# Kernel optimization log

Hardware: AMD Instinct MI355X
Metric: run time of the kernel (lower is better)

Reference implementation:

```python
import jax, jax.numpy as jnp
import numpy as np

KNN = 10       # knn_size
TOPK = 4       # top_k_select
H = 4          # num_heads
HID = 64       # edge-MLP hidden dim


def setup_inputs() -> dict:
    key = jax.random.key(0)
    ks = jax.random.split(key, 12)
    B, V, D = 4, 4096, 256
    s = 0.02
    return {
        "voxel_tokens": jax.random.normal(ks[0], (B, V, D), jnp.float32),
        "voxel_coords": jax.random.uniform(ks[1], (B, V, 3), jnp.float32) * 10.0,
        "mask": jnp.ones((B, V), dtype=bool),
        # EdgeScoringMLP: Linear(2D+3 -> 64), Linear(64 -> 1)
        "W1": jax.random.normal(ks[2], (2 * D + 3, HID), jnp.float32) * s,
        "b1": jnp.zeros((HID,), jnp.float32),
        "W2": jax.random.normal(ks[3], (HID, 1), jnp.float32) * s,
        "b2": jnp.zeros((1,), jnp.float32),
        # CrossAttention projections (D -> D)
        "Wq": jax.random.normal(ks[4], (D, D), jnp.float32) * s,
        "bq": jnp.zeros((D,), jnp.float32),
        "Wk": jax.random.normal(ks[5], (D, D), jnp.float32) * s,
        "bk": jnp.zeros((D,), jnp.float32),
        "Wv": jax.random.normal(ks[6], (D, D), jnp.float32) * s,
        "bv": jnp.zeros((D,), jnp.float32),
        "Wo": jax.random.normal(ks[7], (D, D), jnp.float32) * s,
        "bo": jnp.zeros((D,), jnp.float32),
    }


def reference(voxel_tokens, voxel_coords, mask,
              W1, b1, W2, b2, Wq, bq, Wk, bk, Wv, bv, Wo, bo):
    # mask is all-True (Vp == V per batch element), so the original per-batch
    # loop over dynamic voxel counts is an exact vmap over B. Dropouts are in
    # eval mode (identity).
    D = voxel_tokens.shape[-1]
    Dh = D // H

    def single(tok, coo):  # tok: (V, D), coo: (V, 3)
        # --- KNN graph build (squared euclidean; monotonic in true cdist) ---
        sq = jnp.sum(coo * coo, axis=-1)                        # (V,)
        d2 = sq[:, None] + sq[None, :] - 2.0 * (coo @ coo.T)    # (V, V)
        _, knn = jax.lax.top_k(-d2, KNN + 1)                    # smallest dists
        knn = knn[:, 1:]                                        # drop self, (V, KNN)

        # --- edge features: [anchor_tok, neighbor_tok, rel_pos] ---
        nb_tok = tok[knn]                                       # (V, KNN, D)
        rel = coo[knn] - coo[:, None, :]                        # (V, KNN, 3)
        anchor = jnp.broadcast_to(tok[:, None, :], nb_tok.shape)
        ef = jnp.concatenate([anchor, nb_tok, rel], axis=-1)    # (V, KNN, 2D+3)

        # --- edge-MLP scoring + softmax + top-k edge select ---
        sc = (jax.nn.relu(ef @ W1 + b1) @ W2 + b2)[..., 0]      # (V, KNN)
        aw = jax.nn.softmax(sc, axis=-1)
        _, loc = jax.lax.top_k(aw, TOPK)                        # (V, TOPK)
        sel = jnp.take_along_axis(knn, loc, axis=-1)            # (V, TOPK)
        nbr = tok[sel]                                          # (V, TOPK, D)

        # --- cross attention over selected neighbors ---
        Q = (tok @ Wq + bq).reshape(-1, H, Dh)                  # (V, H, Dh)
        K = (nbr @ Wk + bk).reshape(-1, TOPK, H, Dh)            # (V, TOPK, H, Dh)
        Vv = (nbr @ Wv + bv).reshape(-1, TOPK, H, Dh)
        att = jnp.einsum('vhd,vshd->vhs', Q, K) / jnp.sqrt(jnp.float32(Dh))
        w = jax.nn.softmax(att, axis=-1)                        # (V, H, TOPK)
        out = jnp.einsum('vhs,vshd->vhd', w, Vv).reshape(-1, D)
        return out @ Wo + bo                                    # (V, D)

    return jax.vmap(single)(voxel_tokens, voxel_coords)        # (B, V, D)
```

## Files before the change

### kernel.cpp

```cpp
#include <hip/hip_runtime.h>
#include <hip/hip_bf16.h>

#define VV 4096
#define DDIM 256
#define KNN_K 10
#define TK 4

__device__ __forceinline__ float f_sq3(float x, float y, float z) {
    return __fadd_rn(__fadd_rn(__fmul_rn(x, x), __fmul_rn(y, y)), __fmul_rn(z, z));
}
__device__ __forceinline__ float f_dot3(float ax, float ay, float az,
                                        float bx, float by, float bz) {
    float d = __fmul_rn(ax, bx);
    d = __fmaf_rn(ay, by, d);
    d = __fmaf_rn(az, bz, d);
    return d;
}

__device__ __forceinline__ unsigned long long mkkey(float d2, int j) {
    unsigned u = __float_as_uint(d2);
    u ^= (unsigned)((int)u >> 31) | 0x80000000u;
    return ((unsigned long long)u << 32) | (unsigned)j;
}

__global__ void __launch_bounds__(256) an_gemm_kernel(
    const float* __restrict__ tok,
    const float* __restrict__ W1,
    const float* __restrict__ coords,
    float* __restrict__ AN,
    float4* __restrict__ cxyzs)
{
    __shared__ float As[16][68];
    __shared__ float Bs[16][68];

    const int mBlock = blockIdx.x * 64;
    const int grp    = blockIdx.y;
    const float* W   = W1 + (size_t)grp * 256 * 64;

    const int tid = threadIdx.x;

    if (grp == 0 && tid < 64) {
        int m = mBlock + tid;
        float x = coords[m * 3 + 0], y = coords[m * 3 + 1], z = coords[m * 3 + 2];
        cxyzs[m] = make_float4(x, y, z, f_sq3(x, y, z));
    }

    const int tx = tid & 15;
    const int ty = tid >> 4;

    const int ar  = tid >> 2;
    const int ac4 = tid & 3;
    const int br  = tid >> 4;
    const int bc4 = tid & 15;

    float acc[4][4] = {};

    for (int k0 = 0; k0 < 256; k0 += 16) {
        float4 a4 = *(const float4*)&tok[(size_t)(mBlock + ar) * 256 + k0 + ac4 * 4];
        As[ac4 * 4 + 0][ar] = a4.x;
        As[ac4 * 4 + 1][ar] = a4.y;
        As[ac4 * 4 + 2][ar] = a4.z;
        As[ac4 * 4 + 3][ar] = a4.w;
        float4 b4 = *(const float4*)&W[(size_t)(k0 + br) * 64 + bc4 * 4];
        *(float4*)&Bs[br][bc4 * 4] = b4;
        __syncthreads();
        #pragma unroll
        for (int kk = 0; kk < 16; kk++) {
            float4 av = *(const float4*)&As[kk][ty * 4];
            float4 bv4 = *(const float4*)&Bs[kk][tx * 4];
            acc[0][0] = fmaf(av.x, bv4.x, acc[0][0]); acc[0][1] = fmaf(av.x, bv4.y, acc[0][1]);
            acc[0][2] = fmaf(av.x, bv4.z, acc[0][2]); acc[0][3] = fmaf(av.x, bv4.w, acc[0][3]);
            acc[1][0] = fmaf(av.y, bv4.x, acc[1][0]); acc[1][1] = fmaf(av.y, bv4.y, acc[1][1]);
            acc[1][2] = fmaf(av.y, bv4.z, acc[1][2]); acc[1][3] = fmaf(av.y, bv4.w, acc[1][3]);
            acc[2][0] = fmaf(av.z, bv4.x, acc[2][0]); acc[2][1] = fmaf(av.z, bv4.y, acc[2][1]);
            acc[2][2] = fmaf(av.z, bv4.z, acc[2][2]); acc[2][3] = fmaf(av.z, bv4.w, acc[2][3]);
            acc[3][0] = fmaf(av.w, bv4.x, acc[3][0]); acc[3][1] = fmaf(av.w, bv4.y, acc[3][1]);
            acc[3][2] = fmaf(av.w, bv4.z, acc[3][2]); acc[3][3] = fmaf(av.w, bv4.w, acc[3][3]);
        }
        __syncthreads();
    }

    #pragma unroll
    for (int i = 0; i < 4; i++) {
        int m = mBlock + ty * 4 + i;
        float4 o;
        o.x = acc[i][0]; o.y = acc[i][1]; o.z = acc[i][2]; o.w = acc[i][3];
        *(float4*)&AN[(size_t)m * 128 + grp * 64 + tx * 4] = o;
    }
}

__global__ void __launch_bounds__(256) knn_qkv_kernel(
    const float* __restrict__ AN,
    const float4* __restrict__ cxyzs,
    const float* __restrict__ W1,
    const float* __restrict__ b1,
    const float* __restrict__ W2,
    int* __restrict__ sel,
    const float* __restrict__ tok,
    const float* __restrict__ Wq, const float* __restrict__ bq,
    const float* __restrict__ Wk, const float* __restrict__ bk,
    const float* __restrict__ Wv, const float* __restrict__ bv,
    float* __restrict__ qkv)
{
    __shared__ __align__(16) char smem[16896];
    const int tid   = threadIdx.x;
    const int g     = blockIdx.x;
    const int group = g / 19;
    const int rem   = g - group * 19;

    if (rem < 16) {
        const int kb   = group * 16 + rem;
        const int lane = tid & 63;
        const int wave = tid >> 6;
        const int q    = kb * 4 + wave;
        const int base = q & ~4095;
        const int v    = q & 4095;
        const float4* cx = cxyzs + base;

        int*   sKnn = (int*)smem;
        float* sSc  = (float*)(smem + 160);
        float* sHid = (float*)(smem + 320);

        float4 cq = cx[v];
        const float qx = cq.x, qy = cq.y, qz = cq.z, sqq = cq.w;

        unsigned long long best   = ~0ull;
        unsigned long long second = ~0ull;
        unsigned long long used   = 0ull;

        #pragma unroll 4
        for (int i = 0; i < 64; i++) {
            int j = i * 64 + lane;
            float4 c = cx[j];
            float dt  = f_dot3(qx, qy, qz, c.x, c.y, c.z);
            float d2v = __fsub_rn(__fadd_rn(sqq, c.w), __fmul_rn(2.0f, dt));
            unsigned long long k = mkkey(d2v, j);
            if (k < best) { second = best; best = k; }
            else if (k < second) { second = k; }
        }

        #pragma unroll 1
        for (int it = 0; it < 11; it++) {
            unsigned long long rb = best;
            #pragma unroll
            for (int off = 1; off < 64; off <<= 1) {
                unsigned olo = __shfl_xor((unsigned)rb, off);
                unsigned ohi = __shfl_xor((unsigned)(rb >> 32), off);
                unsigned long long o = ((unsigned long long)ohi << 32) | olo;
                if (o < rb) rb = o;
            }
            int wj = (int)((unsigned)rb & 4095u);
            if (it >= 1 && lane == 0) sKnn[wave * KNN_K + it - 1] = wj;

            if ((unsigned)best == (unsigned)rb) {
                used |= 1ull << (wj >> 6);
                best = second;
                second = ~0ull;
                if (best == ~0ull) {
                    #pragma unroll 1
                    for (int i = 0; i < 64; i++) {
                        if ((used >> i) & 1ull) continue;
                        int j = i * 64 + lane;
                        float4 c = cx[j];
                        float dt  = f_dot3(qx, qy, qz, c.x, c.y, c.z);
                        float d2v = __fsub_rn(__fadd_rn(sqq, c.w), __fmul_rn(2.0f, dt));
                        unsigned long long k = mkkey(d2v, j);
                        if (k < best) { second = best; best = k; }
                        else if (k < second) { second = k; }
                    }
                }
            }
        }

        const float sAl = AN[(size_t)q * 128 + lane];
        const float b1l = b1[lane];
        const float wr0 = W1[(512 + 0) * 64 + lane];
        const float wr1 = W1[(512 + 1) * 64 + lane];
        const float wr2 = W1[(512 + 2) * 64 + lane];

        #pragma unroll 1
        for (int nb = 0; nb < KNN_K; nb++) {
            int kn = sKnn[wave * KNN_K + nb];
            float4 cn = cx[kn];
            float acc = __fadd_rn(sAl, AN[(size_t)(base + kn) * 128 + 64 + lane]);
            float rel0 = __fsub_rn(cn.x, qx);
            acc = __fmaf_rn(rel0, wr0, acc);
            float rel1 = __fsub_rn(cn.y, qy);
            acc = __fmaf_rn(rel1, wr1, acc);
            float rel2 = __fsub_rn(cn.z, qz);
            acc = __fmaf_rn(rel2, wr2, acc);
            float hid = __fadd_rn(acc, b1l);
            sHid[(wave * KNN_K + nb) * 65 + lane] = hid > 0.0f ? hid : 0.0f;
        }

        if (lane < KNN_K) {
            float s = 0.0f;
            #pragma unroll 8
            for (int h = 0; h < 64; h++)
                s = __fmaf_rn(sHid[(wave * KNN_K + lane) * 65 + h], W2[h], s);
            sSc[wave * KNN_K + lane] = s;
        }

        if (lane == 0) {
            unsigned um = 0;
            #pragma unroll
            for (int s = 0; s < TK; s++) {
                float bests = -3.4e38f; int bj = 0;
                for (int jj = 0; jj < KNN_K; jj++) {
                    if (um & (1u << jj)) continue;
                    float sc = sSc[wave * KNN_K + jj];
                    if (sc > bests) { bests = sc; bj = jj; }
                }
                um |= 1u << bj;
                sel[(size_t)q * TK + s] = base + sKnn[wave * KNN_K + bj];
            }
        }
    } else {
        float* As = (float*)smem;
        float* Bs = (float*)smem + 16 * 132;

        const int id     = group * 3 + (rem - 16);
        const int mBlock = (id & 127) * 128;
        const int nb     = id >> 7;
        const int grp    = nb >> 1;
        const int nIn    = (nb & 1) * 128;
        const float* W    = (grp == 0) ? Wq : (grp == 1) ? Wk : Wv;
        const float* bias = (grp == 0) ? bq : (grp == 1) ? bk : bv;

        const int tx = tid & 15;
        const int ty = tid >> 4;
        const int ar  = tid >> 2;
        const int ac4 = tid & 3;
        const int br  = tid >> 4;
        const int bc4 = tid & 15;

        float acc[2][2][4][4] = {};

        for (int k0 = 0; k0 < 256; k0 += 16) {
            float4 a0 = *(const float4*)&tok[(size_t)(mBlock + ar) * 256 + k0 + ac4 * 4];
            float4 a1 = *(const float4*)&tok[(size_t)(mBlock + 64 + ar) * 256 + k0 + ac4 * 4];
            As[(ac4 * 4 + 0) * 132 + ar] = a0.x;      As[(ac4 * 4 + 0) * 132 + 64 + ar] = a1.x;
            As[(ac4 * 4 + 1) * 132 + ar] = a0.y;      As[(ac4 * 4 + 1) * 132 + 64 + ar] = a1.y;
            As[(ac4 * 4 + 2) * 132 + ar] = a0.z;      As[(ac4 * 4 + 2) * 132 + 64 + ar] = a1.z;
            As[(ac4 * 4 + 3) * 132 + ar] = a0.w;      As[(ac4 * 4 + 3) * 132 + 64 + ar] = a1.w;
            float4 b0 = *(const float4*)&W[(size_t)(k0 + br) * 256 + nIn + bc4 * 4];
            float4 b1v = *(const float4*)&W[(size_t)(k0 + br) * 256 + nIn + 64 + bc4 * 4];
            *(float4*)&Bs[br * 132 + bc4 * 4] = b0;
            *(float4*)&Bs[br * 132 + 64 + bc4 * 4] = b1v;
            __syncthreads();
            #pragma unroll
            for (int kk = 0; kk < 16; kk++) {
                float4 av0 = *(const float4*)&As[kk * 132 + ty * 4];
                float4 av1 = *(const float4*)&As[kk * 132 + 64 + ty * 4];
                float4 bv0 = *(const float4*)&Bs[kk * 132 + tx * 4];
                float4 bv1 = *(const float4*)&Bs[kk * 132 + 64 + tx * 4];
                const float am[2][4] = {{av0.x, av0.y, av0.z, av0.w},
                                        {av1.x, av1.y, av1.z, av1.w}};
                const float bn[2][4] = {{bv0.x, bv0.y, bv0.z, bv0.w},
                                        {bv1.x, bv1.y, bv1.z, bv1.w}};
                #pragma unroll
                for (int mi = 0; mi < 2; mi++)
                #pragma unroll
                for (int i = 0; i < 4; i++)
                #pragma unroll
                for (int ni = 0; ni < 2; ni++)
                #pragma unroll
                for (int j = 0; j < 4; j++)
                    acc[mi][ni][i][j] = fmaf(am[mi][i], bn[ni][j], acc[mi][ni][i][j]);
            }
            __syncthreads();
        }

        #pragma unroll
        for (int mi = 0; mi < 2; mi++)
        #pragma unroll
        for (int i = 0; i < 4; i++) {
            int m = mBlock + mi * 64 + ty * 4 + i;
            #pragma unroll
            for (int ni = 0; ni < 2; ni++) {
                int col = nIn + ni * 64 + tx * 4;
                float4 o;
                o.x = acc[mi][ni][i][0] + bias[col + 0];
                o.y = acc[mi][ni][i][1] + bias[col + 1];
                o.z = acc[mi][ni][i][2] + bias[col + 2];
                o.w = acc[mi][ni][i][3] + bias[col + 3];
                *(float4*)&qkv[(size_t)m * 768 + grp * 256 + col] = o;
            }
        }
    }
}

__global__ void __launch_bounds__(256) attn_gather_kernel(
    const float* __restrict__ qkv, const int* __restrict__ sel,
    float* __restrict__ attnout)
{
    const int q = blockIdx.x;
    const int tid = threadIdx.x;

    const float qv = qkv[(size_t)q * 768 + tid];

    int rows[TK];
    #pragma unroll
    for (int s = 0; s < TK; s++) rows[s] = sel[(size_t)q * TK + s];

    float att[TK];
    #pragma unroll
    for (int s = 0; s < TK; s++) {
        float p = qv * qkv[(size_t)rows[s] * 768 + 256 + tid];
        #pragma unroll
        for (int m = 1; m < 64; m <<= 1) p += __shfl_xor(p, m);
        att[s] = p * 0.125f;
    }

    float mx  = fmaxf(fmaxf(att[0], att[1]), fmaxf(att[2], att[3]));
    float e0 = expf(att[0] - mx), e1 = expf(att[1] - mx),
          e2 = expf(att[2] - mx), e3 = expf(att[3] - mx);
    float inv = 1.0f / (e0 + e1 + e2 + e3);

    float o = (e0 * qkv[(size_t)rows[0] * 768 + 512 + tid] +
               e1 * qkv[(size_t)rows[1] * 768 + 512 + tid] +
               e2 * qkv[(size_t)rows[2] * 768 + 512 + tid] +
               e3 * qkv[(size_t)rows[3] * 768 + 512 + tid]) * inv;

    attnout[(size_t)q * 256 + tid] = o;
}

__global__ void __launch_bounds__(256) wo_gemm_kernel(
    const float* __restrict__ A,
    const float* __restrict__ Wo, const float* __restrict__ bo,
    float* __restrict__ out)
{
    __shared__ float As[16][132];
    __shared__ float Bs[16][132];

    const int mBlock = blockIdx.x * 128;
    const int nBlock = blockIdx.y * 128;

    const int tid = threadIdx.x;
    const int tx = tid & 15;
    const int ty = tid >> 4;
    const int ar  = tid >> 2;
    const int ac4 = tid & 3;
    const int br  = tid >> 4;
    const int bc4 = tid & 15;

    float acc[2][2][4][4] = {};

    for (int k0 = 0; k0 < 256; k0 += 16) {
        float4 a0 = *(const float4*)&A[(size_t)(mBlock + ar) * 256 + k0 + ac4 * 4];
        float4 a1 = *(const float4*)&A[(size_t)(mBlock + 64 + ar) * 256 + k0 + ac4 * 4];
        As[ac4 * 4 + 0][ar] = a0.x;      As[ac4 * 4 + 0][64 + ar] = a1.x;
        As[ac4 * 4 + 1][ar] = a0.y;      As[ac4 * 4 + 1][64 + ar] = a1.y;
        As[ac4 * 4 + 2][ar] = a0.z;      As[ac4 * 4 + 2][64 + ar] = a1.z;
        As[ac4 * 4 + 3][ar] = a0.w;      As[ac4 * 4 + 3][64 + ar] = a1.w;
        float4 b0 = *(const float4*)&Wo[(size_t)(k0 + br) * 256 + nBlock + bc4 * 4];
        float4 b1v = *(const float4*)&Wo[(size_t)(k0 + br) * 256 + nBlock + 64 + bc4 * 4];
        *(float4*)&Bs[br][bc4 * 4] = b0;
        *(float4*)&Bs[br][64 + bc4 * 4] = b1v;
        __syncthreads();
        #pragma unroll
        for (int kk = 0; kk < 16; kk++) {
            float4 av0 = *(const float4*)&As[kk][ty * 4];
            float4 av1 = *(const float4*)&As[kk][64 + ty * 4];
            float4 bv0 = *(const float4*)&Bs[kk][tx * 4];
            float4 bv1 = *(const float4*)&Bs[kk][64 + tx * 4];
            const float am[2][4] = {{av0.x, av0.y, av0.z, av0.w},
                                    {av1.x, av1.y, av1.z, av1.w}};
            const float bn[2][4] = {{bv0.x, bv0.y, bv0.z, bv0.w},
                                    {bv1.x, bv1.y, bv1.z, bv1.w}};
            #pragma unroll
            for (int mi = 0; mi < 2; mi++)
            #pragma unroll
            for (int i = 0; i < 4; i++)
            #pragma unroll
            for (int ni = 0; ni < 2; ni++)
            #pragma unroll
            for (int j = 0; j < 4; j++)
                acc[mi][ni][i][j] = fmaf(am[mi][i], bn[ni][j], acc[mi][ni][i][j]);
        }
        __syncthreads();
    }

    #pragma unroll
    for (int mi = 0; mi < 2; mi++)
    #pragma unroll
    for (int i = 0; i < 4; i++) {
        int m = mBlock + mi * 64 + ty * 4 + i;
        #pragma unroll
        for (int ni = 0; ni < 2; ni++) {
            int col = nBlock + ni * 64 + tx * 4;
            float4 o;
            o.x = acc[mi][ni][i][0] + bo[col + 0];
            o.y = acc[mi][ni][i][1] + bo[col + 1];
            o.z = acc[mi][ni][i][2] + bo[col + 2];
            o.w = acc[mi][ni][i][3] + bo[col + 3];
            *(float4*)&out[(size_t)m * 256 + col] = o;
        }
    }
}

__global__ void __launch_bounds__(256) fused_voxel_attn(
    const float* __restrict__ tok,
    const float* __restrict__ coords,
    const float* __restrict__ W1,
    const float* __restrict__ b1,
    const float* __restrict__ W2,
    const float* __restrict__ Wq, const float* __restrict__ bq,
    const float* __restrict__ Wk, const float* __restrict__ bk,
    const float* __restrict__ Wv, const float* __restrict__ bv,
    const float* __restrict__ Wo, const float* __restrict__ bo,
    float* __restrict__ out, int out_size)
{
    const int q    = blockIdx.x;
    const int b    = q >> 12;
    const int v    = q & 4095;
    const int base = q & ~4095;
    const int tid  = threadIdx.x;
    const float* cb = coords + (size_t)b * VV * 3;

    __shared__ float  sval[256];
    __shared__ int    sidx[256];
    __shared__ int    sKnn[KNN_K];
    __shared__ int    sSel[TK];
    __shared__ float  sTokA[DDIM];
    __shared__ float  sTokN[KNN_K][DDIM];
    __shared__ float  sAH[64];
    __shared__ float  sHid[KNN_K][64];
    __shared__ float  sSc[KNN_K];
    __shared__ float  sP[TK][256];
    __shared__ float  sAtt[4][TK];
    __shared__ float  sO[DDIM];

    const float qx = cb[v * 3 + 0];
    const float qy = cb[v * 3 + 1];
    const float qz = cb[v * 3 + 2];
    const float sqq = f_sq3(qx, qy, qz);

    float d2[16];
    #pragma unroll
    for (int i = 0; i < 16; i++) {
        int j = tid + i * 256;
        float xj = cb[j * 3 + 0], yj = cb[j * 3 + 1], zj = cb[j * 3 + 2];
        float sqj = f_sq3(xj, yj, zj);
        float dt  = f_dot3(qx, qy, qz, xj, yj, zj);
        d2[i] = __fsub_rn(__fadd_rn(sqq, sqj), __fmul_rn(2.0f, dt));
    }

    unsigned used = 0;
    for (int it = 0; it < 11; it++) {
        float best = 3.4e38f;
        int bi = 0x7fffffff;
        #pragma unroll
        for (int i = 0; i < 16; i++) {
            if (used & (1u << i)) continue;
            if (d2[i] < best) { best = d2[i]; bi = tid + i * 256; }
        }
        sval[tid] = best;
        sidx[tid] = bi;
        __syncthreads();
        for (int s = 128; s > 0; s >>= 1) {
            if (tid < s) {
                float v2 = sval[tid + s];
                int   i2 = sidx[tid + s];
                if (v2 < sval[tid] || (v2 == sval[tid] && i2 < sidx[tid])) {
                    sval[tid] = v2; sidx[tid] = i2;
                }
            }
            __syncthreads();
        }
        int w = sidx[0] & 4095;
        __syncthreads();
        if (it >= 1 && tid == 0) sKnn[it - 1] = w;
        if ((w & 255) == tid) used |= 1u << (w >> 8);
    }
    __syncthreads();

    sTokA[tid] = tok[(size_t)q * DDIM + tid];
    for (int nb = 0; nb < KNN_K; nb++)
        sTokN[nb][tid] = tok[(size_t)(base + sKnn[nb]) * DDIM + tid];
    __syncthreads();

    if (tid < 64) {
        float a = 0.0f;
        for (int k = 0; k < 256; k++)
            a = __fmaf_rn(sTokA[k], W1[k * 64 + tid], a);
        sAH[tid] = a;
    }
    __syncthreads();

    for (int idx = tid; idx < KNN_K * 64; idx += 256) {
        int nb = idx >> 6;
        int h  = idx & 63;
        float acc = sAH[h];
        const float* tn = sTokN[nb];
        for (int k = 0; k < 256; k++)
            acc = __fmaf_rn(tn[k], W1[(256 + k) * 64 + h], acc);
        #pragma unroll
        for (int c = 0; c < 3; c++) {
            float rel = __fsub_rn(cb[sKnn[nb] * 3 + c], cb[v * 3 + c]);
            acc = __fmaf_rn(rel, W1[(512 + c) * 64 + h], acc);
        }
        float hid = __fadd_rn(acc, b1[h]);
        sHid[nb][h] = hid > 0.0f ? hid : 0.0f;
    }
    __syncthreads();

    if (tid < KNN_K) {
        float s = 0.0f;
        for (int h = 0; h < 64; h++)
            s = __fmaf_rn(sHid[tid][h], W2[h], s);
        sSc[tid] = s;
    }
    __syncthreads();

    if (tid == 0) {
        unsigned um = 0;
        #pragma unroll
        for (int s = 0; s < TK; s++) {
            float best = -3.4e38f; int bj = 0;
            for (int jj = 0; jj < KNN_K; jj++) {
                if (um & (1u << jj)) continue;
                if (sSc[jj] > best) { best = sSc[jj]; bj = jj; }
            }
            um |= 1u << bj;
            sSel[s] = bj;
        }
    }
    __syncthreads();

    int ss[TK];
    float k_acc[TK], v_acc[TK];
    #pragma unroll
    for (int s = 0; s < TK; s++) {
        ss[s] = sSel[s];
        k_acc[s] = bk[tid];
        v_acc[s] = bv[tid];
    }
    float q_acc = bq[tid];

    for (int k = 0; k < 256; k++) {
        float wq = Wq[k * 256 + tid];
        float wk = Wk[k * 256 + tid];
        float wv = Wv[k * 256 + tid];
        q_acc += sTokA[k] * wq;
        #pragma unroll
        for (int s = 0; s < TK; s++) {
            float x = sTokN[ss[s]][k];
            k_acc[s] += x * wk;
            v_acc[s] += x * wv;
        }
    }

    #pragma unroll
    for (int s = 0; s < TK; s++) sP[s][tid] = q_acc * k_acc[s];
    __syncthreads();

    if (tid < 16) {
        int h = tid >> 2, s = tid & 3;
        float p = 0.0f;
        for (int d = 0; d < 64; d++) p += sP[s][h * 64 + d];
        sAtt[h][s] = p * 0.125f;
    }
    __syncthreads();

    const int hh = tid >> 6;
    float a0 = sAtt[hh][0], a1 = sAtt[hh][1], a2 = sAtt[hh][2], a3 = sAtt[hh][3];
    float mx  = fmaxf(fmaxf(a0, a1), fmaxf(a2, a3));
    float e0 = expf(a0 - mx), e1 = expf(a1 - mx), e2 = expf(a2 - mx), e3 = expf(a3 - mx);
    float inv = 1.0f / (e0 + e1 + e2 + e3);
    float o = (e0 * v_acc[0] + e1 * v_acc[1] + e2 * v_acc[2] + e3 * v_acc[3]) * inv;

    sO[tid] = o;
    __syncthreads();

    float a = bo[tid];
    for (int e = 0; e < 256; e++) a += sO[e] * Wo[e * 256 + tid];
    int oidx = q * DDIM + tid;
    if (oidx < out_size)
        out[oidx] = a;
}

extern "C" void kernel_launch(void* const* d_in, const int* in_sizes, int n_in,
                              void* d_out, int out_size, void* d_ws, size_t ws_size,
                              hipStream_t stream)
{
    const long long want[13] = {4194304LL, 49152LL, 32960LL, 64LL, 64LL,
                                65536LL, 256LL, 65536LL, 256LL,
                                65536LL, 256LL, 65536LL, 256LL};
    int idx[13];
    const int n = n_in;

    const long long* s64 = (const long long*)(const void*)in_sizes;
    const int*       s32 = in_sizes;

    bool ok = false;

    if (n >= 13 && s64[0] == want[0]) {
        ok = true;
        int walk = 0;
        for (int t = 0; t < 13; t++) {
            int f = -1;
            for (int i = walk; i < n; i++) {
                if (s64[i] == want[t]) { f = i; break; }
            }
            if (f < 0) { ok = false; break; }
            idx[t] = f; walk = f + 1;
        }
    }

    if (!ok) {
        ok = true;
        int walk = 0;
        for (int t = 0; t < 13; t++) {
            int f = -1;
            for (int i = walk; i < n; i++) {
                if ((long long)s32[i] == want[t]) { f = i; break; }
            }
            if (f < 0) { ok = false; break; }
            idx[t] = f; walk = f + 1;
        }
    }

    if (!ok) return;

    const float* tok    = (const float*)d_in[idx[0]];
    const float* coords = (const float*)d_in[idx[1]];
    const float* W1     = (const float*)d_in[idx[2]];
    const float* b1     = (const float*)d_in[idx[3]];
    const float* W2     = (const float*)d_in[idx[4]];
    const float* Wq     = (const float*)d_in[idx[5]];
    const float* bq     = (const float*)d_in[idx[6]];
    const float* Wk     = (const float*)d_in[idx[7]];
    const float* bk     = (const float*)d_in[idx[8]];
    const float* Wv     = (const float*)d_in[idx[9]];
    const float* bv     = (const float*)d_in[idx[10]];
    const float* Wo     = (const float*)d_in[idx[11]];
    const float* bo     = (const float*)d_in[idx[12]];
    float* out = (float*)d_out;

    const size_t NEED = 67633152;
    if (ws_size >= NEED) {
        char* ws = (char*)d_ws;
        int*    sel     = (int*)   (ws + 0);
        float*  AN      = (float*) (ws + 262144);
        float*  attnout = (float*) (ws + 262144);
        float*  qkv     = (float*) (ws + 17039360);
        float4* cxyzs   = (float4*)(ws + 67371008);

        an_gemm_kernel<<<dim3(256, 2), dim3(256), 0, stream>>>(tok, W1, coords, AN, cxyzs);
        knn_qkv_kernel<<<dim3(4864), dim3(256), 0, stream>>>(
            AN, cxyzs, W1, b1, W2, sel, tok, Wq, bq, Wk, bk, Wv, bv, qkv);
        attn_gather_kernel<<<dim3(16384), dim3(256), 0, stream>>>(qkv, sel, attnout);
        wo_gemm_kernel<<<dim3(128, 2), dim3(256), 0, stream>>>(attnout, Wo, bo, out);
    } else {
        fused_voxel_attn<<<dim3(16384), dim3(256), 0, stream>>>(
            tok, coords, W1, b1, W2, Wq, bq, Wk, bk, Wv, bv, Wo, bo, out, out_size);
    }
}
```

Before: 374.4 us.

## Split fused KNN/QKV kernel into separate launches and pack gather per wave

The combined kernel, which interleaved KNN-scoring blocks with QKV GEMM blocks, is split into a standalone knn_score_kernel and a qkv_gemm_kernel, each launched on its own. The attention gather kernel now handles one query per wave instead of one per block, cutting the block count by four. The GEMM kernels get launch_bounds(256,1) and separate 4x4 accumulator arrays. This removes the mixed-workload scheduling but gives up the overlap between the KNN search and the QKV GEMM, and adds one kernel launch.

```diff
diff --git a/kernel.cpp b/kernel.cpp
--- a/kernel.cpp
+++ b/kernel.cpp
@@ -21,6 +21,17 @@
     unsigned u = __float_as_uint(d2);
     u ^= (unsigned)((int)u >> 31) | 0x80000000u;
     return ((unsigned long long)u << 32) | (unsigned)j;
+}
+
+__device__ __forceinline__ void fma44(const float4 a, const float4 b, float (&c)[4][4]) {
+    c[0][0] = fmaf(a.x, b.x, c[0][0]); c[0][1] = fmaf(a.x, b.y, c[0][1]);
+    c[0][2] = fmaf(a.x, b.z, c[0][2]); c[0][3] = fmaf(a.x, b.w, c[0][3]);
+    c[1][0] = fmaf(a.y, b.x, c[1][0]); c[1][1] = fmaf(a.y, b.y, c[1][1]);
+    c[1][2] = fmaf(a.y, b.z, c[1][2]); c[1][3] = fmaf(a.y, b.w, c[1][3]);
+    c[2][0] = fmaf(a.z, b.x, c[2][0]); c[2][1] = fmaf(a.z, b.y, c[2][1]);
+    c[2][2] = fmaf(a.z, b.z, c[2][2]); c[2][3] = fmaf(a.z, b.w, c[2][3]);
+    c[3][0] = fmaf(a.w, b.x, c[3][0]); c[3][1] = fmaf(a.w, b.y, c[3][1]);
+    c[3][2] = fmaf(a.w, b.z, c[3][2]); c[3][3] = fmaf(a.w, b.w, c[3][3]);
 }
 
 __global__ void __launch_bounds__(256) an_gemm_kernel(
@@ -68,14 +79,7 @@
         for (int kk = 0; kk < 16; kk++) {
             float4 av = *(const float4*)&As[kk][ty * 4];
             float4 bv4 = *(const float4*)&Bs[kk][tx * 4];
-            acc[0][0] = fmaf(av.x, bv4.x, acc[0][0]); acc[0][1] = fmaf(av.x, bv4.y, acc[0][1]);
-            acc[0][2] = fmaf(av.x, bv4.z, acc[0][2]); acc[0][3] = fmaf(av.x, bv4.w, acc[0][3]);
-            acc[1][0] = fmaf(av.y, bv4.x, acc[1][0]); acc[1][1] = fmaf(av.y, bv4.y, acc[1][1]);
-            acc[1][2] = fmaf(av.y, bv4.z, acc[1][2]); acc[1][3] = fmaf(av.y, bv4.w, acc[1][3]);
-            acc[2][0] = fmaf(av.z, bv4.x, acc[2][0]); acc[2][1] = fmaf(av.z, bv4.y, acc[2][1]);
-            acc[2][2] = fmaf(av.z, bv4.z, acc[2][2]); acc[2][3] = fmaf(av.z, bv4.w, acc[2][3]);
-            acc[3][0] = fmaf(av.w, bv4.x, acc[3][0]); acc[3][1] = fmaf(av.w, bv4.y, acc[3][1]);
-            acc[3][2] = fmaf(av.w, bv4.z, acc[3][2]); acc[3][3] = fmaf(av.w, bv4.w, acc[3][3]);
+            fma44(av, bv4, acc);
         }
         __syncthreads();
     }
@@ -89,252 +93,138 @@
     }
 }
 
-__global__ void __launch_bounds__(256) knn_qkv_kernel(
+__global__ void __launch_bounds__(256) knn_score_kernel(
     const float* __restrict__ AN,
     const float4* __restrict__ cxyzs,
     const float* __restrict__ W1,
     const float* __restrict__ b1,
     const float* __restrict__ W2,
-    int* __restrict__ sel,
+    int* __restrict__ sel)
+{
+    const int tid  = threadIdx.x;
+    const int lane = tid & 63;
+    const int wave = tid >> 6;
+    const int q    = blockIdx.x * 4 + wave;
+    const int base = q & ~4095;
+    const int v    = q & 4095;
+    const float4* cx = cxyzs + base;
+
+    __shared__ int   sKnn[4][KNN_K];
+    __shared__ float sSc[4][KNN_K];
+    __shared__ float sHid[4][KNN_K][65];
+
+    float4 cq = cx[v];
+    const float qx = cq.x, qy = cq.y, qz = cq.z, sqq = cq.w;
+
+    unsigned long long best   = ~0ull;
+    unsigned long long second = ~0ull;
+    unsigned long long used   = 0ull;
+
+    #pragma unroll 4
+    for (int i = 0; i < 64; i++) {
+        int j = i * 64 + lane;
+        float4 c = cx[j];
+        float dt  = f_dot3(qx, qy, qz, c.x, c.y, c.z);
+        float d2v = __fsub_rn(__fadd_rn(sqq, c.w), __fmul_rn(2.0f, dt));
+        unsigned long long k = mkkey(d2v, j);
+        if (k < best) { second = best; best = k; }
+        else if (k < second) { second = k; }
+    }
+
+    #pragma unroll 1
+    for (int it = 0; it < 11; it++) {
+        unsigned long long rb = best;
+        #pragma unroll
+        for (int off = 1; off < 64; off <<= 1) {
+            unsigned olo = __shfl_xor((unsigned)rb, off);
+            unsigned ohi = __shfl_xor((unsigned)(rb >> 32), off);
+            unsigned long long o = ((unsigned long long)ohi << 32) | olo;
+            if (o < rb) rb = o;
+        }
+        int wj = (int)((unsigned)rb & 4095u);
+        if (it >= 1 && lane == 0) sKnn[wave][it - 1] = wj;
+
+        if ((unsigned)best == (unsigned)rb) {
+            used |= 1ull << (wj >> 6);
+            best = second;
+            second = ~0ull;
+            if (best == ~0ull) {
+                #pragma unroll 1
+                for (int i = 0; i < 64; i++) {
+                    if ((used >> i) & 1ull) continue;
+                    int j = i * 64 + lane;
+                    float4 c = cx[j];
+                    float dt  = f_dot3(qx, qy, qz, c.x, c.y, c.z);
+                    float d2v = __fsub_rn(__fadd_rn(sqq, c.w), __fmul_rn(2.0f, dt));
+                    unsigned long long k = mkkey(d2v, j);
+                    if (k < best) { second = best; best = k; }
+                    else if (k < second) { second = k; }
+                }
+            }
+        }
+    }
+
+    const float sAl = AN[(size_t)q * 128 + lane];
+    const float b1l = b1[lane];
+    const float wr0 = W1[(512 + 0) * 64 + lane];
+    const float wr1 = W1[(512 + 1) * 64 + lane];
+    const float wr2 = W1[(512 + 2) * 64 + lane];
+
+    #pragma unroll 1
+    for (int nb = 0; nb < KNN_K; nb++) {
+        int kn = sKnn[wave][nb];
+        float4 cn = cx[kn];
+        float acc = __fadd_rn(sAl, AN[(size_t)(base + kn) * 128 + 64 + lane]);
+        float rel0 = __fsub_rn(cn.x, qx);
+        acc = __fmaf_rn(rel0, wr0, acc);
+        float rel1 = __fsub_rn(cn.y, qy);
+        acc = __fmaf_rn(rel1, wr1, acc);
+        float rel2 = __fsub_rn(cn.z, qz);
+        acc = __fmaf_rn(rel2, wr2, acc);
+        float hid = __fadd_rn(acc, b1l);
+        sHid[wave][nb][lane] = hid > 0.0f ? hid : 0.0f;
+    }
+
+    if (lane < KNN_K) {
+        float s = 0.0f;
+        #pragma unroll 8
+        for (int h = 0; h < 64; h++)
+            s = __fmaf_rn(sHid[wave][lane][h], W2[h], s);
+        sSc[wave][lane] = s;
+    }
+
+    if (lane == 0) {
+        unsigned um = 0;
+        #pragma unroll
+        for (int s = 0; s < TK; s++) {
+            float bests = -3.4e38f; int bj = 0;
+            for (int jj = 0; jj < KNN_K; jj++) {
+                if (um & (1u << jj)) continue;
+                float sc = sSc[wave][jj];
+                if (sc > bests) { bests = sc; bj = jj; }
+            }
+            um |= 1u << bj;
+            sel[(size_t)q * TK + s] = base + sKnn[wave][bj];
+        }
+    }
+}
+
+__global__ void __launch_bounds__(256, 1) qkv_gemm_kernel(
     const float* __restrict__ tok,
     const float* __restrict__ Wq, const float* __restrict__ bq,
     const float* __restrict__ Wk, const float* __restrict__ bk,
     const float* __restrict__ Wv, const float* __restrict__ bv,
     float* __restrict__ qkv)
 {
-    __shared__ __align__(16) char smem[16896];
-    const int tid   = threadIdx.x;
-    const int g     = blockIdx.x;
-    const int group = g / 19;
-    const int rem   = g - group * 19;
-
-    if (rem < 16) {
-        const int kb   = group * 16 + rem;
-        const int lane = tid & 63;
-        const int wave = tid >> 6;
-        const int q    = kb * 4 + wave;
-        const int base = q & ~4095;
-        const int v    = q & 4095;
-        const float4* cx = cxyzs + base;
-
-        int*   sKnn = (int*)smem;
-        float* sSc  = (float*)(smem + 160);
-        float* sHid = (float*)(smem + 320);
-
-        float4 cq = cx[v];
-        const float qx = cq.x, qy = cq.y, qz = cq.z, sqq = cq.w;
-
-        unsigned long long best   = ~0ull;
-        unsigned long long second = ~0ull;
-        unsigned long long used   = 0ull;
-
-        #pragma unroll 4
-        for (int i = 0; i < 64; i++) {
-            int j = i * 64 + lane;
-            float4 c = cx[j];
-            float dt  = f_dot3(qx, qy, qz, c.x, c.y, c.z);
-            float d2v = __fsub_rn(__fadd_rn(sqq, c.w), __fmul_rn(2.0f, dt));
-            unsigned long long k = mkkey(d2v, j);
-            if (k < best) { second = best; best = k; }
-            else if (k < second) { second = k; }
-        }
-
-        #pragma unroll 1
-        for (int it = 0; it < 11; it++) {
-            unsigned long long rb = best;
-            #pragma unroll
-            for (int off = 1; off < 64; off <<= 1) {
-                unsigned olo = __shfl_xor((unsigned)rb, off);
-                unsigned ohi = __shfl_xor((unsigned)(rb >> 32), off);
-                unsigned long long o = ((unsigned long long)ohi << 32) | olo;
-                if (o < rb) rb = o;
-            }
-            int wj = (int)((unsigned)rb & 4095u);
-            if (it >= 1 && lane == 0) sKnn[wave * KNN_K + it - 1] = wj;
-
-            if ((unsigned)best == (unsigned)rb) {
-                used |= 1ull << (wj >> 6);
-                best = second;
-                second = ~0ull;
-                if (best == ~0ull) {
-                    #pragma unroll 1
-                    for (int i = 0; i < 64; i++) {
-                        if ((used >> i) & 1ull) continue;
-                        int j = i * 64 + lane;
-                        float4 c = cx[j];
-                        float dt  = f_dot3(qx, qy, qz, c.x, c.y, c.z);
-                        float d2v = __fsub_rn(__fadd_rn(sqq, c.w), __fmul_rn(2.0f, dt));
-                        unsigned long long k = mkkey(d2v, j);
-                        if (k < best) { second = best; best = k; }
-                        else if (k < second) { second = k; }
-                    }
-                }
-            }
-        }
-
-        const float sAl = AN[(size_t)q * 128 + lane];
-        const float b1l = b1[lane];
-        const float wr0 = W1[(512 + 0) * 64 + lane];
-        const float wr1 = W1[(512 + 1) * 64 + lane];
-        const float wr2 = W1[(512 + 2) * 64 + lane];
-
-        #pragma unroll 1
-        for (int nb = 0; nb < KNN_K; nb++) {
-            int kn = sKnn[wave * KNN_K + nb];
-            float4 cn = cx[kn];
-            float acc = __fadd_rn(sAl, AN[(size_t)(base + kn) * 128 + 64 + lane]);
-            float rel0 = __fsub_rn(cn.x, qx);
-            acc = __fmaf_rn(rel0, wr0, acc);
-            float rel1 = __fsub_rn(cn.y, qy);
-            acc = __fmaf_rn(rel1, wr1, acc);
-            float rel2 = __fsub_rn(cn.z, qz);
-            acc = __fmaf_rn(rel2, wr2, acc);
-            float hid = __fadd_rn(acc, b1l);
-            sHid[(wave * KNN_K + nb) * 65 + lane] = hid > 0.0f ? hid : 0.0f;
-        }
-
-        if (lane < KNN_K) {
-            float s = 0.0f;
-            #pragma unroll 8
-            for (int h = 0; h < 64; h++)
-                s = __fmaf_rn(sHid[(wave * KNN_K + lane) * 65 + h], W2[h], s);
-            sSc[wave * KNN_K + lane] = s;
-        }
-
-        if (lane == 0) {
-            unsigned um = 0;
-            #pragma unroll
-            for (int s = 0; s < TK; s++) {
-                float bests = -3.4e38f; int bj = 0;
-                for (int jj = 0; jj < KNN_K; jj++) {
-                    if (um & (1u << jj)) continue;
-                    float sc = sSc[wave * KNN_K + jj];
-                    if (sc > bests) { bests = sc; bj = jj; }
-                }
-                um |= 1u << bj;
-                sel[(size_t)q * TK + s] = base + sKnn[wave * KNN_K + bj];
-            }
-        }
-    } else {
-        float* As = (float*)smem;
-        float* Bs = (float*)smem + 16 * 132;
-
-        const int id     = group * 3 + (rem - 16);
-        const int mBlock = (id & 127) * 128;
-        const int nb     = id >> 7;
-        const int grp    = nb >> 1;
-        const int nIn    = (nb & 1) * 128;
-        const float* W    = (grp == 0) ? Wq : (grp == 1) ? Wk : Wv;
-        const float* bias = (grp == 0) ? bq : (grp == 1) ? bk : bv;
-
-        const int tx = tid & 15;
-        const int ty = tid >> 4;
-        const int ar  = tid >> 2;
-        const int ac4 = tid & 3;
-        const int br  = tid >> 4;
-        const int bc4 = tid & 15;
-
-        float acc[2][2][4][4] = {};
-
-        for (int k0 = 0; k0 < 256; k0 += 16) {
-            float4 a0 = *(const float4*)&tok[(size_t)(mBlock + ar) * 256 + k0 + ac4 * 4];
-            float4 a1 = *(const float4*)&tok[(size_t)(mBlock + 64 + ar) * 256 + k0 + ac4 * 4];
-            As[(ac4 * 4 + 0) * 132 + ar] = a0.x;      As[(ac4 * 4 + 0) * 132 + 64 + ar] = a1.x;
-            As[(ac4 * 4 + 1) * 132 + ar] = a0.y;      As[(ac4 * 4 + 1) * 132 + 64 + ar] = a1.y;
-            As[(ac4 * 4 + 2) * 132 + ar] = a0.z;      As[(ac4 * 4 + 2) * 132 + 64 + ar] = a1.z;
-            As[(ac4 * 4 + 3) * 132 + ar] = a0.w;      As[(ac4 * 4 + 3) * 132 + 64 + ar] = a1.w;
-            float4 b0 = *(const float4*)&W[(size_t)(k0 + br) * 256 + nIn + bc4 * 4];
-            float4 b1v = *(const float4*)&W[(size_t)(k0 + br) * 256 + nIn + 64 + bc4 * 4];
-            *(float4*)&Bs[br * 132 + bc4 * 4] = b0;
-            *(float4*)&Bs[br * 132 + 64 + bc4 * 4] = b1v;
-            __syncthreads();
-            #pragma unroll
-            for (int kk = 0; kk < 16; kk++) {
-                float4 av0 = *(const float4*)&As[kk * 132 + ty * 4];
-                float4 av1 = *(const float4*)&As[kk * 132 + 64 + ty * 4];
-                float4 bv0 = *(const float4*)&Bs[kk * 132 + tx * 4];
-                float4 bv1 = *(const float4*)&Bs[kk * 132 + 64 + tx * 4];
-                const float am[2][4] = {{av0.x, av0.y, av0.z, av0.w},
-                                        {av1.x, av1.y, av1.z, av1.w}};
-                const float bn[2][4] = {{bv0.x, bv0.y, bv0.z, bv0.w},
-                                        {bv1.x, bv1.y, bv1.z, bv1.w}};
-                #pragma unroll
-                for (int mi = 0; mi < 2; mi++)
-                #pragma unroll
-                for (int i = 0; i < 4; i++)
-                #pragma unroll
-                for (int ni = 0; ni < 2; ni++)
-                #pragma unroll
-                for (int j = 0; j < 4; j++)
-                    acc[mi][ni][i][j] = fmaf(am[mi][i], bn[ni][j], acc[mi][ni][i][j]);
-            }
-            __syncthreads();
-        }
-
-        #pragma unroll
-        for (int mi = 0; mi < 2; mi++)
-        #pragma unroll
-        for (int i = 0; i < 4; i++) {
-            int m = mBlock + mi * 64 + ty * 4 + i;
-            #pragma unroll
-            for (int ni = 0; ni < 2; ni++) {
-                int col = nIn + ni * 64 + tx * 4;
-                float4 o;
-                o.x = acc[mi][ni][i][0] + bias[col + 0];
-                o.y = acc[mi][ni][i][1] + bias[col + 1];
-                o.z = acc[mi][ni][i][2] + bias[col + 2];
-                o.w = acc[mi][ni][i][3] + bias[col + 3];
-                *(float4*)&qkv[(size_t)m * 768 + grp * 256 + col] = o;
-            }
-        }
-    }
-}
-
-__global__ void __launch_bounds__(256) attn_gather_kernel(
-    const float* __restrict__ qkv, const int* __restrict__ sel,
-    float* __restrict__ attnout)
-{
-    const int q = blockIdx.x;
-    const int tid = threadIdx.x;
-
-    const float qv = qkv[(size_t)q * 768 + tid];
-
-    int rows[TK];
-    #pragma unroll
-    for (int s = 0; s < TK; s++) rows[s] = sel[(size_t)q * TK + s];
-
-    float att[TK];
-    #pragma unroll
-    for (int s = 0; s < TK; s++) {
-        float p = qv * qkv[(size_t)rows[s] * 768 + 256 + tid];
-        #pragma unroll
-        for (int m = 1; m < 64; m <<= 1) p += __shfl_xor(p, m);
-        att[s] = p * 0.125f;
-    }
-
-    float mx  = fmaxf(fmaxf(att[0], att[1]), fmaxf(att[2], att[3]));
-    float e0 = expf(att[0] - mx), e1 = expf(att[1] - mx),
-          e2 = expf(att[2] - mx), e3 = expf(att[3] - mx);
-    float inv = 1.0f / (e0 + e1 + e2 + e3);
-
-    float o = (e0 * qkv[(size_t)rows[0] * 768 + 512 + tid] +
-               e1 * qkv[(size_t)rows[1] * 768 + 512 + tid] +
-               e2 * qkv[(size_t)rows[2] * 768 + 512 + tid] +
-               e3 * qkv[(size_t)rows[3] * 768 + 512 + tid]) * inv;
-
-    attnout[(size_t)q * 256 + tid] = o;
-}
-
-__global__ void __launch_bounds__(256) wo_gemm_kernel(
-    const float* __restrict__ A,
-    const float* __restrict__ Wo, const float* __restrict__ bo,
-    float* __restrict__ out)
-{
     __shared__ float As[16][132];
     __shared__ float Bs[16][132];
 
     const int mBlock = blockIdx.x * 128;
-    const int nBlock = blockIdx.y * 128;
+    const int nb     = blockIdx.y;
+    const int grp    = nb >> 1;
+    const int nIn    = (nb & 1) * 128;
+    const float* W    = (grp == 0) ? Wq : (grp == 1) ? Wk : Wv;
+    const float* bias = (grp == 0) ? bq : (grp == 1) ? bk : bv;
 
     const int tid = threadIdx.x;
     const int tx = tid & 15;
@@ -344,7 +234,119 @@
     const int br  = tid >> 4;
     const int bc4 = tid & 15;
 
-    float acc[2][2][4][4] = {};
+    float acc00[4][4] = {}, acc01[4][4] = {}, acc10[4][4] = {}, acc11[4][4] = {};
+
+    for (int k0 = 0; k0 < 256; k0 += 16) {
+        float4 a0 = *(const float4*)&tok[(size_t)(mBlock + ar) * 256 + k0 + ac4 * 4];
+        float4 a1 = *(const float4*)&tok[(size_t)(mBlock + 64 + ar) * 256 + k0 + ac4 * 4];
+        As[ac4 * 4 + 0][ar] = a0.x;      As[ac4 * 4 + 0][64 + ar] = a1.x;
+        As[ac4 * 4 + 1][ar] = a0.y;      As[ac4 * 4 + 1][64 + ar] = a1.y;
+        As[ac4 * 4 + 2][ar] = a0.z;      As[ac4 * 4 + 2][64 + ar] = a1.z;
+        As[ac4 * 4 + 3][ar] = a0.w;      As[ac4 * 4 + 3][64 + ar] = a1.w;
+        float4 b0 = *(const float4*)&W[(size_t)(k0 + br) * 256 + nIn + bc4 * 4];
+        float4 b1v = *(const float4*)&W[(size_t)(k0 + br) * 256 + nIn + 64 + bc4 * 4];
+        *(float4*)&Bs[br][bc4 * 4] = b0;
+        *(float4*)&Bs[br][64 + bc4 * 4] = b1v;
+        __syncthreads();
+        #pragma unroll
+        for (int kk = 0; kk < 16; kk++) {
+            float4 av0 = *(const float4*)&As[kk][ty * 4];
+            float4 av1 = *(const float4*)&As[kk][64 + ty * 4];
+            float4 bv0 = *(const float4*)&Bs[kk][tx * 4];
+            float4 bv1 = *(const float4*)&Bs[kk][64 + tx * 4];
+            fma44(av0, bv0, acc00);
+            fma44(av0, bv1, acc01);
+            fma44(av1, bv0, acc10);
+            fma44(av1, bv1, acc11);
+        }
+        __syncthreads();
+    }
+
+    #pragma unroll
+    for (int i = 0; i < 4; i++) {
+        int m0 = mBlock + ty * 4 + i;
+        int m1 = m0 + 64;
+        int c0 = nIn + tx * 4;
+        int c1 = c0 + 64;
+        float4 o;
+        o.x = acc00[i][0] + bias[c0 + 0]; o.y = acc00[i][1] + bias[c0 + 1];
+        o.z = acc00[i][2] + bias[c0 + 2]; o.w = acc00[i][3] + bias[c0 + 3];
+        *(float4*)&qkv[(size_t)m0 * 768 + grp * 256 + c0] = o;
+        o.x = acc01[i][0] + bias[c1 + 0]; o.y = acc01[i][1] + bias[c1 + 1];
+        o.z = acc01[i][2] + bias[c1 + 2]; o.w = acc01[i][3] + bias[c1 + 3];
+        *(float4*)&qkv[(size_t)m0 * 768 + grp * 256 + c1] = o;
+        o.x = acc10[i][0] + bias[c0 + 0]; o.y = acc10[i][1] + bias[c0 + 1];
+        o.z = acc10[i][2] + bias[c0 + 2]; o.w = acc10[i][3] + bias[c0 + 3];
+        *(float4*)&qkv[(size_t)m1 * 768 + grp * 256 + c0] = o;
+        o.x = acc11[i][0] + bias[c1 + 0]; o.y = acc11[i][1] + bias[c1 + 1];
+        o.z = acc11[i][2] + bias[c1 + 2]; o.w = acc11[i][3] + bias[c1 + 3];
+        *(float4*)&qkv[(size_t)m1 * 768 + grp * 256 + c1] = o;
+    }
+}
+
+__global__ void __launch_bounds__(256) attn_gather_kernel(
+    const float* __restrict__ qkv, const int* __restrict__ sel,
+    float* __restrict__ attnout)
+{
+    const int tid  = threadIdx.x;
+    const int lane = tid & 63;
+    const int wave = tid >> 6;
+    const int q    = blockIdx.x * 4 + wave;
+
+    int rows[TK];
+    #pragma unroll
+    for (int s = 0; s < TK; s++) rows[s] = sel[(size_t)q * TK + s];
+
+    const float* qrow = qkv + (size_t)q * 768;
+
+    #pragma unroll
+    for (int h = 0; h < 4; h++) {
+        const int d = h * 64 + lane;
+        const float qv = qrow[d];
+
+        float att[TK];
+        #pragma unroll
+        for (int s = 0; s < TK; s++) {
+            float p = qv * qkv[(size_t)rows[s] * 768 + 256 + d];
+            #pragma unroll
+            for (int m = 1; m < 64; m <<= 1) p += __shfl_xor(p, m);
+            att[s] = p * 0.125f;
+        }
+
+        float mx  = fmaxf(fmaxf(att[0], att[1]), fmaxf(att[2], att[3]));
+        float e0 = expf(att[0] - mx), e1 = expf(att[1] - mx),
+              e2 = expf(att[2] - mx), e3 = expf(att[3] - mx);
+        float inv = 1.0f / (e0 + e1 + e2 + e3);
+
+        float o = (e0 * qkv[(size_t)rows[0] * 768 + 512 + d] +
+                   e1 * qkv[(size_t)rows[1] * 768 + 512 + d] +
+                   e2 * qkv[(size_t)rows[2] * 768 + 512 + d] +
+                   e3 * qkv[(size_t)rows[3] * 768 + 512 + d]) * inv;
+
+        attnout[(size_t)q * 256 + d] = o;
+    }
+}
+
+__global__ void __launch_bounds__(256, 1) wo_gemm_kernel(
+    const float* __restrict__ A,
+    const float* __restrict__ Wo, const float* __restrict__ bo,
+    float* __restrict__ out)
+{
+    __shared__ float As[16][132];
+    __shared__ float Bs[16][132];
+
+    const int mBlock = blockIdx.x * 128;
+    const int nBlock = blockIdx.y * 128;
+
+    const int tid = threadIdx.x;
+    const int tx = tid & 15;
+    const int ty = tid >> 4;
+    const int ar  = tid >> 2;
+    const int ac4 = tid & 3;
+    const int br  = tid >> 4;
+    const int bc4 = tid & 15;
+
+    float acc00[4][4] = {}, acc01[4][4] = {}, acc10[4][4] = {}, acc11[4][4] = {};
 
     for (int k0 = 0; k0 < 256; k0 += 16) {
         float4 a0 = *(const float4*)&A[(size_t)(mBlock + ar) * 256 + k0 + ac4 * 4];
@@ -364,38 +366,33 @@
             float4 av1 = *(const float4*)&As[kk][64 + ty * 4];
             float4 bv0 = *(const float4*)&Bs[kk][tx * 4];
             float4 bv1 = *(const float4*)&Bs[kk][64 + tx * 4];
-            const float am[2][4] = {{av0.x, av0.y, av0.z, av0.w},
-                                    {av1.x, av1.y, av1.z, av1.w}};
-            const float bn[2][4] = {{bv0.x, bv0.y, bv0.z, bv0.w},
-                                    {bv1.x, bv1.y, bv1.z, bv1.w}};
-            #pragma unroll
-            for (int mi = 0; mi < 2; mi++)
-            #pragma unroll
-            for (int i = 0; i < 4; i++)
-            #pragma unroll
-            for (int ni = 0; ni < 2; ni++)
-            #pragma unroll
-            for (int j = 0; j < 4; j++)
-                acc[mi][ni][i][j] = fmaf(am[mi][i], bn[ni][j], acc[mi][ni][i][j]);
-        }
-        __syncthreads();
-    }
-
-    #pragma unroll
-    for (int mi = 0; mi < 2; mi++)
+            fma44(av0, bv0, acc00);
+            fma44(av0, bv1, acc01);
+            fma44(av1, bv0, acc10);
+            fma44(av1, bv1, acc11);
+        }
+        __syncthreads();
+    }
+
     #pragma unroll
     for (int i = 0; i < 4; i++) {
-        int m = mBlock + mi * 64 + ty * 4 + i;
-        #pragma unroll
-        for (int ni = 0; ni < 2; ni++) {
-            int col = nBlock + ni * 64 + tx * 4;
-            float4 o;
-            o.x = acc[mi][ni][i][0] + bo[col + 0];
-            o.y = acc[mi][ni][i][1] + bo[col + 1];
-            o.z = acc[mi][ni][i][2] + bo[col + 2];
-            o.w = acc[mi][ni][i][3] + bo[col + 3];
-            *(float4*)&out[(size_t)m * 256 + col] = o;
-        }
+        int m0 = mBlock + ty * 4 + i;
+        int m1 = m0 + 64;
+        int c0 = nBlock + tx * 4;
+        int c1 = c0 + 64;
+        float4 o;
+        o.x = acc00[i][0] + bo[c0 + 0]; o.y = acc00[i][1] + bo[c0 + 1];
+        o.z = acc00[i][2] + bo[c0 + 2]; o.w = acc00[i][3] + bo[c0 + 3];
+        *(float4*)&out[(size_t)m0 * 256 + c0] = o;
+        o.x = acc01[i][0] + bo[c1 + 0]; o.y = acc01[i][1] + bo[c1 + 1];
+        o.z = acc01[i][2] + bo[c1 + 2]; o.w = acc01[i][3] + bo[c1 + 3];
+        *(float4*)&out[(size_t)m0 * 256 + c1] = o;
+        o.x = acc10[i][0] + bo[c0 + 0]; o.y = acc10[i][1] + bo[c0 + 1];
+        o.z = acc10[i][2] + bo[c0 + 2]; o.w = acc10[i][3] + bo[c0 + 3];
+        *(float4*)&out[(size_t)m1 * 256 + c0] = o;
+        o.x = acc11[i][0] + bo[c1 + 0]; o.y = acc11[i][1] + bo[c1 + 1];
+        o.z = acc11[i][2] + bo[c1 + 2]; o.w = acc11[i][3] + bo[c1 + 3];
+        *(float4*)&out[(size_t)m1 * 256 + c1] = o;
     }
 }
 
@@ -648,9 +645,9 @@
         float4* cxyzs   = (float4*)(ws + 67371008);
 
         an_gemm_kernel<<<dim3(256, 2), dim3(256), 0, stream>>>(tok, W1, coords, AN, cxyzs);
-        knn_qkv_kernel<<<dim3(4864), dim3(256), 0, stream>>>(
-            AN, cxyzs, W1, b1, W2, sel, tok, Wq, bq, Wk, bk, Wv, bv, qkv);
-        attn_gather_kernel<<<dim3(16384), dim3(256), 0, stream>>>(qkv, sel, attnout);
+        knn_score_kernel<<<dim3(4096), dim3(256), 0, stream>>>(AN, cxyzs, W1, b1, W2, sel);
+        qkv_gemm_kernel<<<dim3(128, 6), dim3(256), 0, stream>>>(tok, Wq, bq, Wk, bk, Wv, bv, qkv);
+        attn_gather_kernel<<<dim3(4096), dim3(256), 0, stream>>>(qkv, sel, attnout);
         wo_gemm_kernel<<<dim3(128, 2), dim3(256), 0, stream>>>(attnout, Wo, bo, out);
     } else {
         fused_voxel_attn<<<dim3(16384), dim3(256), 0, stream>>>(
```

Result: no change. 367.2 us (-1.9%).
